# Optimization experiments

Hardware: AMD Instinct MI355X
Metric: run time of the kernel (lower is better)

## Reference

```python
import jax, jax.numpy as jnp
import numpy as np

D_MODEL = 2816
N_EXPERTS = 64
TOP_K = 8
RMS_EPS = 1e-6


def setup_inputs() -> dict:
    key = jax.random.key(0)
    k1, k2, k3, k4 = jax.random.split(key, 4)
    x = jax.random.normal(k1, (8, 4096, D_MODEL), dtype=jnp.float32)
    W = jax.random.normal(k2, (N_EXPERTS, D_MODEL), dtype=jnp.float32) * (D_MODEL ** -0.5)
    scale = jax.random.uniform(k3, (D_MODEL,), dtype=jnp.float32)
    per_expert_scale = jax.random.uniform(k4, (N_EXPERTS,), dtype=jnp.float32)
    return {"x": x, "W": W, "scale": scale, "per_expert_scale": per_expert_scale}


def reference(x, W, scale, per_expert_scale):
    # RMSNorm (no learned scale in norm itself)
    v = jnp.mean(jnp.square(x), axis=-1, keepdims=True)
    h = x * jax.lax.rsqrt(v + RMS_EPS)
    # elementwise scale + 1/sqrt(d)
    h = h * scale * (D_MODEL ** -0.5)
    # tiny projection to expert logits: [B,S,E]
    scores = jnp.einsum('bsd,ed->bse', h, W)
    prob = jax.nn.softmax(scores, axis=-1)
    topw, topi = jax.lax.top_k(prob, TOP_K)          # [B,S,K]
    topw = topw / jnp.sum(topw, axis=-1, keepdims=True)
    topw = topw * per_expert_scale[topi]
    # one-hot scatter back to dense [B,S,E]
    oh = jax.nn.one_hot(topi, N_EXPERTS, dtype=topw.dtype)  # [B,S,K,E]
    return jnp.einsum('bsk,bske->bse', topw, oh)
```

## Files before the change

### kernel.cpp

```cpp
#include <hip/hip_runtime.h>
#include <math.h>
#include <float.h>

#define D_MODEL 2816
#define N_EXP   64
#define TOPK    8
#define T_TILE  64
#define DC      32
#define NCHUNK  88
#define SROW    36
#define SMEM_BYTES 18688
#define TAU     3e-4f


__global__ __launch_bounds__(256, 2)
void router_a(const float* __restrict__ x,
              const float* __restrict__ W,
              const float* __restrict__ scale,
              const float* __restrict__ pes,
              float* __restrict__ out,
              unsigned int* __restrict__ cnt,
              int* __restrict__ list,
              int cap)
{
    __shared__ __align__(16) char smem[SMEM_BYTES];
    float (*xs)[SROW] = (float (*)[SROW])(smem);
    float (*ws)[SROW] = (float (*)[SROW])(smem + 9216);
    float* raw  = (float*)smem;
    float* ssqp = (float*)(smem + 16384);
    float* rn   = (float*)(smem + 18432);

    const int tid  = threadIdx.x;
    const int tb   = blockIdx.x * T_TILE;
    const int lrow = tid >> 3;
    const int kk   = tid & 7;
    const int tg4  = (tid >> 4) << 2;
    const int eg   = tid & 15;

    float acc[4][4] = {};
    float ssq2[2] = {0.f, 0.f};

    for (int c = 0; c < NCHUNK; ++c) {
        const int d0 = c * DC;
        float4 xg[2], wg[2];
        const float4 sc4 = *(const float4*)(scale + d0 + kk * 4);
        #pragma unroll
        for (int r = 0; r < 2; ++r) {
            const int row = r * 32 + lrow;
            xg[r] = *(const float4*)(x + (size_t)(tb + row) * D_MODEL + d0 + kk * 4);
            wg[r] = *(const float4*)(W + (size_t)row * D_MODEL + d0 + kk * 4);
        }
        __syncthreads();
        #pragma unroll
        for (int r = 0; r < 2; ++r) {
            const int row = r * 32 + lrow;
            ssq2[r] += xg[r].x * xg[r].x + xg[r].y * xg[r].y
                     + xg[r].z * xg[r].z + xg[r].w * xg[r].w;
            *(float4*)&xs[row][kk * 4] = xg[r];
            float4 wv;
            wv.x = wg[r].x * sc4.x; wv.y = wg[r].y * sc4.y;
            wv.z = wg[r].z * sc4.z; wv.w = wg[r].w * sc4.w;
            *(float4*)&ws[row][kk * 4] = wv;
        }
        __syncthreads();
        #pragma unroll
        for (int d = 0; d < DC; d += 4) {
            float4 xf[4], wf[4];
            #pragma unroll
            for (int u = 0; u < 4; ++u)
                xf[u] = *(const float4*)&xs[tg4 + u][d];
            #pragma unroll
            for (int v = 0; v < 4; ++v)
                wf[v] = *(const float4*)&ws[eg + 16 * v][d];
            #pragma unroll
            for (int u = 0; u < 4; ++u)
                #pragma unroll
                for (int v = 0; v < 4; ++v) {
                    acc[u][v] = fmaf(xf[u].x, wf[v].x, acc[u][v]);
                    acc[u][v] = fmaf(xf[u].y, wf[v].y, acc[u][v]);
                    acc[u][v] = fmaf(xf[u].z, wf[v].z, acc[u][v]);
                    acc[u][v] = fmaf(xf[u].w, wf[v].w, acc[u][v]);
                }
        }
    }

    __syncthreads();

    #pragma unroll
    for (int u = 0; u < 4; ++u)
        #pragma unroll
        for (int v = 0; v < 4; ++v)
            raw[(tg4 + u) * 64 + (eg + 16 * v)] = acc[u][v];
    ssqp[lrow * 8 + kk]        = ssq2[0];
    ssqp[(32 + lrow) * 8 + kk] = ssq2[1];
    __syncthreads();

    if (tid < 64) {
        float s = 0.f;
        #pragma unroll
        for (int j = 0; j < 8; ++j) s += ssqp[tid * 8 + j];
        float v  = s + 0.002816f;
        float r0 = rsqrtf(v);
        r0 = r0 * (1.5f - 0.5f * v * r0 * r0);
        rn[tid] = r0;
    }
    __syncthreads();

    const int wv = tid >> 6, lane = tid & 63;
    const float pl = pes[lane];
    for (int tk = 0; tk < 16; ++tk) {
        const int t = wv * 16 + tk;
        const float sraw = raw[t * 64 + lane];
        float m = sraw;
        int rank = 0;
        for (int j = 0; j < 64; ++j) {
            float sj = raw[t * 64 + j];
            rank += (sj > sraw) || (sj == sraw && j < lane);
        }
        const bool sel = rank < TOPK;
        float a = sel ?  sraw :  FLT_MAX;
        float b = sel ? -FLT_MAX :  sraw;
        #pragma unroll
        for (int off = 32; off > 0; off >>= 1) {
            m = fmaxf(m, __shfl_xor(m, off));
            a = fminf(a, __shfl_xor(a, off));
            b = fmaxf(b, __shfl_xor(b, off));
        }
        const float rt = rn[t];
        float ex = sel ? __expf((sraw - m) * rt) : 0.f;
        float sum = ex;
        #pragma unroll
        for (int off = 32; off > 0; off >>= 1) sum += __shfl_xor(sum, off);
        out[(size_t)(tb + t) * N_EXP + lane] = sel ? (ex / sum) * pl : 0.f;
        if (lane == 0 && (a - b) < TAU) {
            unsigned int slot = atomicAdd(cnt, 1u);
            if ((int)slot < cap) list[slot] = tb + t;
        }
    }
}

__global__ __launch_bounds__(256, 2)
void router_b(const float* __restrict__ x,
              const float* __restrict__ W,
              const float* __restrict__ scale,
              const float* __restrict__ pes,
              float* __restrict__ out,
              const unsigned int* __restrict__ cnt,
              const int* __restrict__ list,
              int cap)
{
    __shared__ double part[256];
    __shared__ double sc[64];
    __shared__ double qsh[4];

    const int tid = threadIdx.x;
    const int e   = tid & 63;
    const int seg = tid >> 6;
    int n = (int)*cnt;
    if (n > cap) n = cap;

    for (int i = blockIdx.x; i < n; i += gridDim.x) {
        const int t = list[i];
        const float* xr = x + (size_t)t * D_MODEL;
        const float* wr = W + (size_t)e * D_MODEL;
        double s = 0.0, q = 0.0;
        const int dbeg = seg * 704;
        for (int d = dbeg; d < dbeg + 704; d += 4) {
            float4 xv = *(const float4*)(xr + d);
            float4 wvv = *(const float4*)(wr + d);
            float4 sv = *(const float4*)(scale + d);
            s += (double)xv.x * ((double)sv.x * (double)wvv.x)
               + (double)xv.y * ((double)sv.y * (double)wvv.y)
               + (double)xv.z * ((double)sv.z * (double)wvv.z)
               + (double)xv.w * ((double)sv.w * (double)wvv.w);
            if (e == 0)
                q += (double)xv.x * xv.x + (double)xv.y * xv.y
                   + (double)xv.z * xv.z + (double)xv.w * xv.w;
        }
        part[tid] = s;
        if (e == 0) qsh[seg] = q;
        __syncthreads();
        if (tid < 64)
            sc[tid] = part[tid] + part[tid + 64] + part[tid + 128] + part[tid + 192];
        __syncthreads();
        if (tid < 64) {
            const int lane = tid;
            const double sraw = sc[lane];
            double m = sraw;
            #pragma unroll
            for (int off = 32; off > 0; off >>= 1) {
                double o = __shfl_xor(m, off);
                m = m > o ? m : o;
            }
            int rank = 0;
            for (int j = 0; j < 64; ++j) {
                double sj = sc[j];
                rank += (sj > sraw) || (sj == sraw && j < lane);
            }
            const bool sel = rank < TOPK;
            float ssqf = (float)(qsh[0] + qsh[1] + qsh[2] + qsh[3]);
            float v  = ssqf + 0.002816f;
            float r0 = rsqrtf(v);
            r0 = r0 * (1.5f - 0.5f * v * r0 * r0);
            float ex = sel ? __expf((float)(sraw - m) * r0) : 0.f;
            float sum = ex;
            #pragma unroll
            for (int off = 32; off > 0; off >>= 1) sum += __shfl_xor(sum, off);
            out[(size_t)t * N_EXP + lane] = sel ? (ex / sum) * pes[lane] : 0.f;
        }
        __syncthreads();
    }
}

extern "C" void kernel_launch(void* const* d_in, const int* in_sizes, int n_in,
                              void* d_out, int out_size, void* d_ws, size_t ws_size,
                              hipStream_t stream) {
    const float* x     = (const float*)d_in[0];
    const float* W     = (const float*)d_in[1];
    const float* scale = (const float*)d_in[2];
    const float* pes   = (const float*)d_in[3];
    float* out = (float*)d_out;

    unsigned int* cnt = (unsigned int*)d_ws;
    int* list = (int*)((char*)d_ws + 16);
    long cap_l = ((long)ws_size - 16) / 4;
    int cap = cap_l < 0 ? 0 : (cap_l > 32768 ? 32768 : (int)cap_l);

    const int ntok    = in_sizes[0] / D_MODEL;
    const int nblocks = ntok / T_TILE;

    hipMemsetAsync(d_ws, 0, 16, stream);
    router_a<<<dim3(nblocks), dim3(256), 0, stream>>>(x, W, scale, pes, out, cnt, list, cap);
    router_b<<<dim3(128), dim3(256), 0, stream>>>(x, W, scale, pes, out, cnt, list, cap);
}
```

Before: 736.3 us.

## Use split-bf16 MFMA for router logits with register prefetch of next chunk

Replaces the FP32 FMA inner product in the router kernel with bf16 MFMA (16x16x32) using a hi/lo split of x and scaled W, taking three MFMAs per tile to approximate FP32 accuracy. It also prefetches the next chunk's x, W and scale into registers before the shared-memory store, so the global loads overlap with compute. The tie threshold for the double-precision fallback is widened to cover the bf16 error, which can send more tokens to router_b, and router_b's grid is raised to 192 blocks. The cost is some precision in the logits and possibly more fallback work.

After: 689.3 us. 6.4% less time.

```diff
diff --git a/kernel.cpp b/kernel.cpp
--- a/kernel.cpp
+++ b/kernel.cpp
@@ -8,10 +8,29 @@
 #define T_TILE  64
 #define DC      32
 #define NCHUNK  88
-#define SROW    36
-#define SMEM_BYTES 18688
-#define TAU     3e-4f
-
+#define AROW    40
+#define TAU_RAW 1e-3f
+#define SMEM_BYTES 20480
+
+typedef __attribute__((ext_vector_type(8))) short short8;
+typedef __attribute__((ext_vector_type(4))) float f32x4;
+
+
+__device__ inline ushort bf16_rn(float f) {
+    unsigned u = __float_as_uint(f);
+    unsigned r = u + 0x7FFFu + ((u >> 16) & 1u);
+    return (ushort)(r >> 16);
+}
+
+__device__ inline void split4(float4 f, ushort4& h, ushort4& l) {
+    ushort h0 = bf16_rn(f.x), h1 = bf16_rn(f.y), h2 = bf16_rn(f.z), h3 = bf16_rn(f.w);
+    float r0 = f.x - __uint_as_float((unsigned)h0 << 16);
+    float r1 = f.y - __uint_as_float((unsigned)h1 << 16);
+    float r2 = f.z - __uint_as_float((unsigned)h2 << 16);
+    float r3 = f.w - __uint_as_float((unsigned)h3 << 16);
+    h = make_ushort4(h0, h1, h2, h3);
+    l = make_ushort4(bf16_rn(r0), bf16_rn(r1), bf16_rn(r2), bf16_rn(r3));
+}
 
 __global__ __launch_bounds__(256, 2)
 void router_a(const float* __restrict__ x,
@@ -24,81 +43,123 @@
               int cap)
 {
     __shared__ __align__(16) char smem[SMEM_BYTES];
-    float (*xs)[SROW] = (float (*)[SROW])(smem);
-    float (*ws)[SROW] = (float (*)[SROW])(smem + 9216);
-    float* raw  = (float*)smem;
-    float* ssqp = (float*)(smem + 16384);
-    float* rn   = (float*)(smem + 18432);
-
-    const int tid  = threadIdx.x;
-    const int tb   = blockIdx.x * T_TILE;
-    const int lrow = tid >> 3;
-    const int kk   = tid & 7;
-    const int tg4  = (tid >> 4) << 2;
-    const int eg   = tid & 15;
-
-    float acc[4][4] = {};
-    float ssq2[2] = {0.f, 0.f};
+    ushort* xs_hi = (ushort*)smem;
+    ushort* xs_lo = xs_hi + 2560;
+    ushort* wb_hi = xs_lo + 2560;
+    ushort* wb_lo = wb_hi + 2560;
+    float*  raw   = (float*)smem;
+    float*  ssqp  = (float*)(smem + 16384);
+    float*  rn    = (float*)(smem + 17408);
+
+    const int tid = threadIdx.x;
+    const int tb  = blockIdx.x * T_TILE;
+    const int row = tid >> 2;
+    const int q   = tid & 3;
+    const int c0  = 4 * q;
+    const int w   = tid >> 6;
+    const int l   = tid & 63;
+    const int lm  = l & 15;
+    const int kg  = (l >> 4) * 8;
+
+    const size_t xrow_base = (size_t)(tb + row) * D_MODEL;
+    const size_t wrow_base = (size_t)row * D_MODEL;
+
+    f32x4 acc0 = {0.f,0.f,0.f,0.f}, acc1 = {0.f,0.f,0.f,0.f};
+    f32x4 acc2 = {0.f,0.f,0.f,0.f}, acc3 = {0.f,0.f,0.f,0.f};
+    float sq = 0.f;
+
+    float4 xg0 = *(const float4*)(x + xrow_base + c0);
+    float4 xg1 = *(const float4*)(x + xrow_base + c0 + 16);
+    float4 wg0 = *(const float4*)(W + wrow_base + c0);
+    float4 wg1 = *(const float4*)(W + wrow_base + c0 + 16);
+    float4 sg0 = *(const float4*)(scale + c0);
+    float4 sg1 = *(const float4*)(scale + c0 + 16);
 
     for (int c = 0; c < NCHUNK; ++c) {
-        const int d0 = c * DC;
-        float4 xg[2], wg[2];
-        const float4 sc4 = *(const float4*)(scale + d0 + kk * 4);
+        sq += xg0.x*xg0.x + xg0.y*xg0.y + xg0.z*xg0.z + xg0.w*xg0.w
+            + xg1.x*xg1.x + xg1.y*xg1.y + xg1.z*xg1.z + xg1.w*xg1.w;
+        ushort4 xh0, xl0, xh1, xl1, wh0, wl0, wh1, wl1;
+        split4(xg0, xh0, xl0);
+        split4(xg1, xh1, xl1);
+        float4 ws0 = make_float4(wg0.x*sg0.x, wg0.y*sg0.y, wg0.z*sg0.z, wg0.w*sg0.w);
+        float4 ws1 = make_float4(wg1.x*sg1.x, wg1.y*sg1.y, wg1.z*sg1.z, wg1.w*sg1.w);
+        split4(ws0, wh0, wl0);
+        split4(ws1, wh1, wl1);
+
+        const int d0n = (c + 1 < NCHUNK ? c + 1 : NCHUNK - 1) * DC;
+        xg0 = *(const float4*)(x + xrow_base + d0n + c0);
+        xg1 = *(const float4*)(x + xrow_base + d0n + c0 + 16);
+        wg0 = *(const float4*)(W + wrow_base + d0n + c0);
+        wg1 = *(const float4*)(W + wrow_base + d0n + c0 + 16);
+        sg0 = *(const float4*)(scale + d0n + c0);
+        sg1 = *(const float4*)(scale + d0n + c0 + 16);
+
+        __syncthreads();
+        const int rb = row * AROW;
+        *(ushort4*)(xs_hi + rb + c0)      = xh0;
+        *(ushort4*)(xs_hi + rb + c0 + 16) = xh1;
+        *(ushort4*)(xs_lo + rb + c0)      = xl0;
+        *(ushort4*)(xs_lo + rb + c0 + 16) = xl1;
+        *(ushort4*)(wb_hi + rb + c0)      = wh0;
+        *(ushort4*)(wb_hi + rb + c0 + 16) = wh1;
+        *(ushort4*)(wb_lo + rb + c0)      = wl0;
+        *(ushort4*)(wb_lo + rb + c0 + 16) = wl1;
+        __syncthreads();
+
+        const int abase = (16 * w + lm) * AROW + kg;
+        short8 ahi = *(const short8*)(xs_hi + abase);
+        short8 alo = *(const short8*)(xs_lo + abase);
+        {
+            const int b0 = (lm) * AROW + kg;
+            short8 bhi = *(const short8*)(wb_hi + b0);
+            short8 blo = *(const short8*)(wb_lo + b0);
+            acc0 = __builtin_amdgcn_mfma_f32_16x16x32_bf16(ahi, bhi, acc0, 0, 0, 0);
+            acc0 = __builtin_amdgcn_mfma_f32_16x16x32_bf16(ahi, blo, acc0, 0, 0, 0);
+            acc0 = __builtin_amdgcn_mfma_f32_16x16x32_bf16(alo, bhi, acc0, 0, 0, 0);
+        }
+        {
+            const int b1 = (16 + lm) * AROW + kg;
+            short8 bhi = *(const short8*)(wb_hi + b1);
+            short8 blo = *(const short8*)(wb_lo + b1);
+            acc1 = __builtin_amdgcn_mfma_f32_16x16x32_bf16(ahi, bhi, acc1, 0, 0, 0);
+            acc1 = __builtin_amdgcn_mfma_f32_16x16x32_bf16(ahi, blo, acc1, 0, 0, 0);
+            acc1 = __builtin_amdgcn_mfma_f32_16x16x32_bf16(alo, bhi, acc1, 0, 0, 0);
+        }
+        {
+            const int b2 = (32 + lm) * AROW + kg;
+            short8 bhi = *(const short8*)(wb_hi + b2);
+            short8 blo = *(const short8*)(wb_lo + b2);
+            acc2 = __builtin_amdgcn_mfma_f32_16x16x32_bf16(ahi, bhi, acc2, 0, 0, 0);
+            acc2 = __builtin_amdgcn_mfma_f32_16x16x32_bf16(ahi, blo, acc2, 0, 0, 0);
+            acc2 = __builtin_amdgcn_mfma_f32_16x16x32_bf16(alo, bhi, acc2, 0, 0, 0);
+        }
+        {
+            const int b3 = (48 + lm) * AROW + kg;
+            short8 bhi = *(const short8*)(wb_hi + b3);
+            short8 blo = *(const short8*)(wb_lo + b3);
+            acc3 = __builtin_amdgcn_mfma_f32_16x16x32_bf16(ahi, bhi, acc3, 0, 0, 0);
+            acc3 = __builtin_amdgcn_mfma_f32_16x16x32_bf16(ahi, blo, acc3, 0, 0, 0);
+            acc3 = __builtin_amdgcn_mfma_f32_16x16x32_bf16(alo, bhi, acc3, 0, 0, 0);
+        }
+    }
+
+    __syncthreads();
+
+    {
+        const int trow = 16 * w + (l >> 4) * 4;
         #pragma unroll
-        for (int r = 0; r < 2; ++r) {
-            const int row = r * 32 + lrow;
-            xg[r] = *(const float4*)(x + (size_t)(tb + row) * D_MODEL + d0 + kk * 4);
-            wg[r] = *(const float4*)(W + (size_t)row * D_MODEL + d0 + kk * 4);
-        }
-        __syncthreads();
-        #pragma unroll
-        for (int r = 0; r < 2; ++r) {
-            const int row = r * 32 + lrow;
-            ssq2[r] += xg[r].x * xg[r].x + xg[r].y * xg[r].y
-                     + xg[r].z * xg[r].z + xg[r].w * xg[r].w;
-            *(float4*)&xs[row][kk * 4] = xg[r];
-            float4 wv;
-            wv.x = wg[r].x * sc4.x; wv.y = wg[r].y * sc4.y;
-            wv.z = wg[r].z * sc4.z; wv.w = wg[r].w * sc4.w;
-            *(float4*)&ws[row][kk * 4] = wv;
-        }
-        __syncthreads();
-        #pragma unroll
-        for (int d = 0; d < DC; d += 4) {
-            float4 xf[4], wf[4];
-            #pragma unroll
-            for (int u = 0; u < 4; ++u)
-                xf[u] = *(const float4*)&xs[tg4 + u][d];
-            #pragma unroll
-            for (int v = 0; v < 4; ++v)
-                wf[v] = *(const float4*)&ws[eg + 16 * v][d];
-            #pragma unroll
-            for (int u = 0; u < 4; ++u)
-                #pragma unroll
-                for (int v = 0; v < 4; ++v) {
-                    acc[u][v] = fmaf(xf[u].x, wf[v].x, acc[u][v]);
-                    acc[u][v] = fmaf(xf[u].y, wf[v].y, acc[u][v]);
-                    acc[u][v] = fmaf(xf[u].z, wf[v].z, acc[u][v]);
-                    acc[u][v] = fmaf(xf[u].w, wf[v].w, acc[u][v]);
-                }
-        }
-    }
-
+        for (int r = 0; r < 4; ++r) {
+            raw[(trow + r) * 64 +      lm] = acc0[r];
+            raw[(trow + r) * 64 + 16 + lm] = acc1[r];
+            raw[(trow + r) * 64 + 32 + lm] = acc2[r];
+            raw[(trow + r) * 64 + 48 + lm] = acc3[r];
+        }
+    }
+    ssqp[row * 4 + q] = sq;
     __syncthreads();
 
-    #pragma unroll
-    for (int u = 0; u < 4; ++u)
-        #pragma unroll
-        for (int v = 0; v < 4; ++v)
-            raw[(tg4 + u) * 64 + (eg + 16 * v)] = acc[u][v];
-    ssqp[lrow * 8 + kk]        = ssq2[0];
-    ssqp[(32 + lrow) * 8 + kk] = ssq2[1];
-    __syncthreads();
-
     if (tid < 64) {
-        float s = 0.f;
-        #pragma unroll
-        for (int j = 0; j < 8; ++j) s += ssqp[tid * 8 + j];
+        float s = ssqp[tid*4] + ssqp[tid*4+1] + ssqp[tid*4+2] + ssqp[tid*4+3];
         float v  = s + 0.002816f;
         float r0 = rsqrtf(v);
         r0 = r0 * (1.5f - 0.5f * v * r0 * r0);
@@ -132,7 +193,7 @@
         #pragma unroll
         for (int off = 32; off > 0; off >>= 1) sum += __shfl_xor(sum, off);
         out[(size_t)(tb + t) * N_EXP + lane] = sel ? (ex / sum) * pl : 0.f;
-        if (lane == 0 && (a - b) < TAU) {
+        if (lane == 0 && (a - b) < TAU_RAW) {
             unsigned int slot = atomicAdd(cnt, 1u);
             if ((int)slot < cap) list[slot] = tb + t;
         }
@@ -163,7 +224,7 @@
         const int t = list[i];
         const float* xr = x + (size_t)t * D_MODEL;
         const float* wr = W + (size_t)e * D_MODEL;
-        double s = 0.0, q = 0.0;
+        double s = 0.0, qq = 0.0;
         const int dbeg = seg * 704;
         for (int d = dbeg; d < dbeg + 704; d += 4) {
             float4 xv = *(const float4*)(xr + d);
@@ -174,11 +235,11 @@
                + (double)xv.z * ((double)sv.z * (double)wvv.z)
                + (double)xv.w * ((double)sv.w * (double)wvv.w);
             if (e == 0)
-                q += (double)xv.x * xv.x + (double)xv.y * xv.y
-                   + (double)xv.z * xv.z + (double)xv.w * xv.w;
+                qq += (double)xv.x * xv.x + (double)xv.y * xv.y
+                    + (double)xv.z * xv.z + (double)xv.w * xv.w;
         }
         part[tid] = s;
-        if (e == 0) qsh[seg] = q;
+        if (e == 0) qsh[seg] = qq;
         __syncthreads();
         if (tid < 64)
             sc[tid] = part[tid] + part[tid + 64] + part[tid + 128] + part[tid + 192];
@@ -231,5 +292,5 @@
 
     hipMemsetAsync(d_ws, 0, 16, stream);
     router_a<<<dim3(nblocks), dim3(256), 0, stream>>>(x, W, scale, pes, out, cnt, list, cap);
-    router_b<<<dim3(128), dim3(256), 0, stream>>>(x, W, scale, pes, out, cnt, list, cap);
-}
+    router_b<<<dim3(192), dim3(256), 0, stream>>>(x, W, scale, pes, out, cnt, list, cap);
+}
```
